# Kernel tuning notes

Hardware: AMD Instinct MI355X
Metric: run time of the kernel (lower is better)

## Reference

```python
import jax, jax.numpy as jnp
import numpy as np

N_NODES = 100000
N_EDGES = 3200000
IN_F = 128


def gcn_conv(x, edge_index, edge_weight, W, b):
    """PyG GCNConv: add self-loops (weight 1), symmetric normalization,
    scatter-add aggregation from src -> dst, then bias."""
    n = x.shape[0]
    src, dst = edge_index[0], edge_index[1]
    h = x @ W  # [N, out]
    # degree with self-loop weight 1
    deg = jax.ops.segment_sum(edge_weight, dst, num_segments=n) + 1.0
    dinv = jax.lax.rsqrt(deg)
    norm = dinv[src] * edge_weight * dinv[dst]  # [E]
    msgs = norm[:, None] * h[src]  # [E, out]
    out = jax.ops.segment_sum(msgs, dst, num_segments=n)
    # self-loop contribution: norm = dinv*1*dinv = 1/deg
    out = out + h / deg[:, None]
    return out + b


def setup_inputs() -> dict:
    key = jax.random.key(0)
    ks = jax.random.split(key, 12)
    x = jax.random.normal(ks[0], (N_NODES, IN_F), dtype=jnp.float32)
    edge_index = jax.random.randint(ks[1], (2, N_EDGES), 0, N_NODES)
    edge_weights = jax.random.uniform(ks[2], (N_EDGES,), dtype=jnp.float32)
    def glorot(k, shape):
        lim = np.sqrt(6.0 / (shape[0] + shape[1]))
        return jax.random.uniform(k, shape, jnp.float32, -lim, lim)
    return {
        "x": x,
        "edge_index": edge_index,
        "edge_weights": edge_weights,
        "W1": glorot(ks[3], (IN_F, 32)),
        "b1": jnp.zeros((32,), jnp.float32),
        "W2": glorot(ks[4], (32, 16)),
        "b2": jnp.zeros((16,), jnp.float32),
        "fc1_w": glorot(ks[5], (16, 1)),
        "fc1_b": jnp.zeros((1,), jnp.float32),
        "fc2_w": glorot(ks[6], (33, 1)),
        "fc2_b": jnp.zeros((1,), jnp.float32),
    }


def reference(x, edge_index, edge_weights, W1, b1, W2, b2, fc1_w, fc1_b, fc2_w, fc2_b):
    x1 = gcn_conv(x, edge_index, edge_weights, W1, b1)
    h = jax.nn.relu(x1)  # dropout is identity in eval mode
    x2 = gcn_conv(h, edge_index, edge_weights, W2, b2)
    x1f = x2 @ fc1_w + fc1_b        # [N, 1]
    c = jax.nn.sigmoid(x1f)
    cat = jnp.concatenate([h, c], axis=1)  # [N, 33]
    r = cat @ fc2_w + fc2_b         # [N, 1]
    return (r, x1f)
```

## Files before the change

kernel.cpp:

```cpp
#include <hip/hip_runtime.h>
#include <math.h>


#define TPB 256
#define PA_CHUNK 4096
#define KMAXB 512
#define NPW 8

__global__ __launch_bounds__(512) void countA_kernel(const int* __restrict__ dst,
                                                     int* __restrict__ gtot,
                                                     int E, int K) {
    __shared__ int lhist[KMAXB];
    const int tid = threadIdx.x;
    const int e0  = blockIdx.x * PA_CHUNK;
    if (tid < KMAXB) lhist[tid] = 0;
    __syncthreads();
#pragma unroll
    for (int i = 0; i < 8; ++i) {
        int e = e0 + tid + i * 512;
        if (e < E) atomicAdd(&lhist[dst[e] >> 8], 1);
    }
    __syncthreads();
    if (tid < K && lhist[tid] > 0) atomicAdd(&gtot[tid], lhist[tid]);
}

__global__ __launch_bounds__(64) void kscan_kernel(const int* __restrict__ gtot,
                                                   int* __restrict__ gstart,
                                                   int* __restrict__ gcursor,
                                                   int K, int E) {
    int tid = threadIdx.x;
    int b0 = tid * 8, v[8], s = 0;
#pragma unroll
    for (int t = 0; t < 8; ++t) {
        v[t] = s;
        int idx = b0 + t;
        s += (idx < K) ? gtot[idx] : 0;
    }
    int incl = s;
#pragma unroll
    for (int d = 1; d < 64; d <<= 1) {
        int t2 = __shfl_up(incl, d);
        if (tid >= d) incl += t2;
    }
    int excl = incl - s;
#pragma unroll
    for (int t = 0; t < 8; ++t) {
        int idx = b0 + t;
        if (idx < K) { gstart[idx] = excl + v[t]; gcursor[idx] = excl + v[t]; }
    }
    if (tid == 63) gstart[K] = E;
}

__global__ __launch_bounds__(512) void placeA_kernel(const int* __restrict__ src,
                                                     const int* __restrict__ dst,
                                                     const float* __restrict__ ew,
                                                     uint2* __restrict__ tmp,
                                                     int* __restrict__ gcursor,
                                                     int E, int K) {
    __shared__ int lhist[KMAXB], lbase[KMAXB], lcur[KMAXB], gbaseS[KMAXB];
    __shared__ int ltot;
    __shared__ uint2 stage[PA_CHUNK];
    __shared__ int   saddr[PA_CHUNK];
    const int tid = threadIdx.x;
    const int e0  = blockIdx.x * PA_CHUNK;

    if (tid < KMAXB) { lhist[tid] = 0; lcur[tid] = 0; }
    __syncthreads();

    int   b[8];
    uint2 p[8];
#pragma unroll
    for (int i = 0; i < 8; ++i) {
        int e = e0 + tid + i * 512;
        b[i] = -1;
        if (e < E) {
            int d   = dst[e];
            int s   = src[e];
            float w = ew[e];
            b[i]   = d >> 8;
            p[i].x = __float_as_uint(w);
            p[i].y = ((unsigned)s << 8) | (unsigned)(d & 255);
            atomicAdd(&lhist[b[i]], 1);
        }
    }
    __syncthreads();

    if (tid < 64) {
        int b0 = tid * 8, v[8], s = 0;
#pragma unroll
        for (int t = 0; t < 8; ++t) { v[t] = s; s += lhist[b0 + t]; }
        int incl = s;
#pragma unroll
        for (int d = 1; d < 64; d <<= 1) {
            int t2 = __shfl_up(incl, d);
            if (tid >= d) incl += t2;
        }
        int excl = incl - s;
#pragma unroll
        for (int t = 0; t < 8; ++t) lbase[b0 + t] = excl + v[t];
        if (tid == 63) ltot = incl;
    }
    __syncthreads();

    if (tid < K && lhist[tid] > 0)
        gbaseS[tid] = atomicAdd(&gcursor[tid], lhist[tid]);
    __syncthreads();

#pragma unroll
    for (int i = 0; i < 8; ++i) {
        if (b[i] >= 0) {
            int r    = atomicAdd(&lcur[b[i]], 1);
            int sidx = lbase[b[i]] + r;
            stage[sidx] = p[i];
            saddr[sidx] = gbaseS[b[i]] + r;
        }
    }
    __syncthreads();

    int tot = ltot;
    for (int s = tid; s < tot; s += 512) tmp[saddr[s]] = stage[s];
}

__global__ __launch_bounds__(512) void partB_kernel(const uint2* __restrict__ tmp,
                                                    const int* __restrict__ gstart,
                                                    int2* __restrict__ epair,
                                                    int* __restrict__ off,
                                                    float* __restrict__ dinv,
                                                    int N) {
    __shared__ int   lhist[256], loff[256], lcur[256];
    __shared__ float ldeg[256];
    const int tid  = threadIdx.x;
    const int k    = blockIdx.x;
    const int seg0 = gstart[k], seg1 = gstart[k + 1];

    if (tid < 256) { lhist[tid] = 0; lcur[tid] = 0; ldeg[tid] = 0.f; }
    __syncthreads();

    for (int j = seg0 + tid; j < seg1; j += 512)
        atomicAdd(&lhist[tmp[j].y & 255u], 1);
    __syncthreads();

    if (tid < 64) {
        int b0 = tid * 4, v[4], s = 0;
#pragma unroll
        for (int t = 0; t < 4; ++t) { v[t] = s; s += lhist[b0 + t]; }
        int incl = s;
#pragma unroll
        for (int d = 1; d < 64; d <<= 1) {
            int t2 = __shfl_up(incl, d);
            if (tid >= d) incl += t2;
        }
        int excl = incl - s;
#pragma unroll
        for (int t = 0; t < 4; ++t) loff[b0 + t] = excl + v[t];
    }
    __syncthreads();

    if (tid < 256) {
        int d = (k << 8) + tid;
        if (d < N) off[d] = seg0 + loff[tid];
    }

    for (int j = seg0 + tid; j < seg1; j += 512) {
        uint2 q  = tmp[j];
        int dlow = q.y & 255u;
        int s    = (int)(q.y >> 8);
        float w  = __uint_as_float(q.x);
        int r    = atomicAdd(&lcur[dlow], 1);
        int2 pr; pr.x = s; pr.y = (int)q.x;
        epair[seg0 + loff[dlow] + r] = pr;
        atomicAdd(&ldeg[dlow], w);
    }
    __syncthreads();

    if (tid < 256) {
        int d = (k << 8) + tid;
        if (d < N) dinv[d] = 1.0f / sqrtf(ldeg[tid] + 1.0f);
    }
}

__global__ __launch_bounds__(TPB) void gemm1_kernel(const float* __restrict__ x,
                                                    const float* __restrict__ W,
                                                    const float* __restrict__ dinv,
                                                    float* __restrict__ h, int N) {
    __shared__ float Ws[128 * 32];
    __shared__ float xs[32 * 129];
    const int tid = threadIdx.x;
    const int nb  = blockIdx.x * 32;

    const float4* W4  = (const float4*)W;
    float4*       Ws4 = (float4*)Ws;
#pragma unroll
    for (int i = 0; i < 4; ++i) Ws4[tid + i * 256] = W4[tid + i * 256];

#pragma unroll
    for (int i = 0; i < 4; ++i) {
        int idx  = tid + i * 256;
        int node = idx >> 5;
        int col4 = idx & 31;
        if (nb + node < N) {
            float4 v = ((const float4*)(x + (size_t)nb * 128))[idx];
            float* p = &xs[node * 129 + col4 * 4];
            p[0] = v.x; p[1] = v.y; p[2] = v.z; p[3] = v.w;
        }
    }
    __syncthreads();

    const int nl = tid >> 3;
    const int og = (tid & 7) * 4;
    float a0 = 0.f, a1 = 0.f, a2 = 0.f, a3 = 0.f;
#pragma unroll 8
    for (int k = 0; k < 128; ++k) {
        float xv = xs[nl * 129 + k];
        const float* wp = &Ws[k * 32 + og];
        a0 = fmaf(xv, wp[0], a0);
        a1 = fmaf(xv, wp[1], a1);
        a2 = fmaf(xv, wp[2], a2);
        a3 = fmaf(xv, wp[3], a3);
    }
    int node = nb + nl;
    if (node < N) {
        float dv = dinv[node];
        float* out = &h[(size_t)node * 32 + og];
        out[0] = a0 * dv; out[1] = a1 * dv; out[2] = a2 * dv; out[3] = a3 * dv;
    }
}

__global__ __launch_bounds__(TPB) void gather32_fused_kernel(
    const int* __restrict__ off, const int2* __restrict__ epair,
    const float* __restrict__ g1, const float* __restrict__ dinv,
    const float* __restrict__ b1, const float* __restrict__ W2,
    const float* __restrict__ fc2_w,
    float* __restrict__ g2, float* __restrict__ rdot, int N, int E) {
    __shared__ float wls[544];
    const int tid = threadIdx.x;
    wls[tid]       = W2[tid];
    wls[tid + 256] = W2[tid + 256];
    if (tid < 32) wls[512 + tid] = fc2_w[tid];
    __syncthreads();

    const int lane = tid & 63;
    const int f    = lane & 31;
    const int half = lane >> 5;
    const float bv = b1[f];
    const int wbase = (lane < 16) ? lane : 512;
    const int wstrd = (lane < 16) ? 16 : 1;

    const int i0 = (blockIdx.x * (TPB / 64) + (tid >> 6)) * NPW;

    for (int t = 0; t < NPW; ++t) {
        int i = i0 + t;
        if (i >= N) return;
        const int s0 = off[i];
        const int s1 = (i + 1 < N) ? off[i + 1] : E;

        float acc = 0.f;
        int j = s0 + half;
        for (; j + 6 < s1; j += 8) {
            int2 pa = epair[j];
            int2 pb = epair[j + 2];
            int2 pc = epair[j + 4];
            int2 pd = epair[j + 6];
            acc = fmaf(__int_as_float(pa.y), g1[(size_t)pa.x * 32 + f], acc);
            acc = fmaf(__int_as_float(pb.y), g1[(size_t)pb.x * 32 + f], acc);
            acc = fmaf(__int_as_float(pc.y), g1[(size_t)pc.x * 32 + f], acc);
            acc = fmaf(__int_as_float(pd.y), g1[(size_t)pd.x * 32 + f], acc);
        }
        for (; j < s1; j += 2) {
            int2 p = epair[j];
            acc = fmaf(__int_as_float(p.y), g1[(size_t)p.x * 32 + f], acc);
        }
        acc += __shfl_xor(acc, 32);

        float dv = dinv[i];
        float v  = fmaxf(dv * (acc + g1[(size_t)i * 32 + f]) + bv, 0.f);

        float hs = 0.f;
#pragma unroll
        for (int k = 0; k < 32; ++k)
            hs = fmaf(__shfl(v, k), wls[wbase + k * wstrd], hs);

        if (lane < 16)       g2[(size_t)i * 16 + lane] = hs * dv;
        else if (lane == 16) rdot[i] = hs;
    }
}

__global__ __launch_bounds__(TPB) void zprep_kernel(const float* __restrict__ g2,
                                                    const float* __restrict__ fc1_w,
                                                    float* __restrict__ z, int N) {
    int i = blockIdx.x * TPB + threadIdx.x;
    if (i >= N) return;
    const float4* g4 = (const float4*)(g2 + (size_t)i * 16);
    float acc = 0.f;
#pragma unroll
    for (int q = 0; q < 4; ++q) {
        float4 v = g4[q];
        acc = fmaf(v.x, fc1_w[q * 4 + 0], acc);
        acc = fmaf(v.y, fc1_w[q * 4 + 1], acc);
        acc = fmaf(v.z, fc1_w[q * 4 + 2], acc);
        acc = fmaf(v.w, fc1_w[q * 4 + 3], acc);
    }
    z[i] = acc;
}

__global__ __launch_bounds__(TPB) void final_scalar_kernel(
    const int* __restrict__ off, const int2* __restrict__ epair,
    const float* __restrict__ z, const float* __restrict__ rdot,
    const float* __restrict__ dinv, const float* __restrict__ b2,
    const float* __restrict__ fc1_w, const float* __restrict__ fc1_b,
    const float* __restrict__ fc2_w, const float* __restrict__ fc2_b,
    float* __restrict__ out, int N, int E) {
    const int tid  = threadIdx.x;
    const int lane = tid & 63;

    float C = fc1_b[0];
#pragma unroll
    for (int f = 0; f < 16; ++f) C = fmaf(b2[f], fc1_w[f], C);
    const float f2w = fc2_w[32];
    const float f2b = fc2_b[0];

    const int i0 = (blockIdx.x * (TPB / 64) + (tid >> 6)) * NPW;

    for (int t = 0; t < NPW; ++t) {
        int i = i0 + t;
        if (i >= N) return;
        const int s0 = off[i];
        const int s1 = (i + 1 < N) ? off[i + 1] : E;

        float acc = 0.f;
        for (int j = s0 + lane; j < s1; j += 64) {
            int2 p = epair[j];
            acc = fmaf(__int_as_float(p.y), z[p.x], acc);
        }
        acc += __shfl_xor(acc, 1);
        acc += __shfl_xor(acc, 2);
        acc += __shfl_xor(acc, 4);
        acc += __shfl_xor(acc, 8);
        acc += __shfl_xor(acc, 16);
        acc += __shfl_xor(acc, 32);

        float x1f = dinv[i] * (acc + z[i]) + C;
        float c   = 1.0f / (1.0f + expf(-x1f));
        float r   = fmaf(c, f2w, f2b) + rdot[i];

        if (lane == 0) {
            out[i]     = r;
            out[N + i] = x1f;
        }
    }
}

extern "C" void kernel_launch(void* const* d_in, const int* in_sizes, int n_in,
                              void* d_out, int out_size, void* d_ws, size_t ws_size,
                              hipStream_t stream) {
    const float* x     = (const float*)d_in[0];
    const int*   ei    = (const int*)d_in[1];
    const float* ew    = (const float*)d_in[2];
    const float* W1    = (const float*)d_in[3];
    const float* b1    = (const float*)d_in[4];
    const float* W2    = (const float*)d_in[5];
    const float* b2    = (const float*)d_in[6];
    const float* fc1_w = (const float*)d_in[7];
    const float* fc1_b = (const float*)d_in[8];
    const float* fc2_w = (const float*)d_in[9];
    const float* fc2_b = (const float*)d_in[10];

    const int N = in_sizes[0] / 128;
    const int E = in_sizes[2];
    const int* src = ei;
    const int* dst = ei + E;
    const int K = (N + 255) >> 8;

    float* ws    = (float*)d_ws;
    float* dinv  = ws;
    float* big   = dinv + N;
    float* g1    = big;
    float* g2    = big + (size_t)32 * N;
    float* rdot  = big + (size_t)48 * N;
    float* z     = big + (size_t)49 * N;
    int*   off   = (int*)(big + (size_t)64 * N);
    int2*  epair = (int2*)(off + N);
    int*   gcursor = (int*)(epair + E);
    int*   gstart  = gcursor + K;
    uint2* tmp   = (uint2*)big;

    size_t need = ((size_t)66 * N + (size_t)2 * E + 2 * K + 2) * 4;
    if (ws_size < need || K > KMAXB || (size_t)E > (size_t)32 * N) return;

    hipMemsetAsync(gcursor, 0, (size_t)K * sizeof(int), stream);

    countA_kernel<<<(E + PA_CHUNK - 1) / PA_CHUNK, 512, 0, stream>>>(dst, gcursor, E, K);
    kscan_kernel<<<1, 64, 0, stream>>>(gcursor, gstart, gcursor, K, E);
    placeA_kernel<<<(E + PA_CHUNK - 1) / PA_CHUNK, 512, 0, stream>>>(
        src, dst, ew, tmp, gcursor, E, K);
    partB_kernel<<<K, 512, 0, stream>>>(tmp, gstart, epair, off, dinv, N);

    gemm1_kernel<<<(N + 31) / 32, TPB, 0, stream>>>(x, W1, dinv, g1, N);

    const int gblocks = (N + 4 * NPW - 1) / (4 * NPW);
    gather32_fused_kernel<<<gblocks, TPB, 0, stream>>>(
        off, epair, g1, dinv, b1, W2, fc2_w, g2, rdot, N, E);
    zprep_kernel<<<(N + TPB - 1) / TPB, TPB, 0, stream>>>(g2, fc1_w, z, N);
    final_scalar_kernel<<<gblocks, TPB, 0, stream>>>(
        off, epair, z, rdot, dinv, b2, fc1_w, fc1_b, fc2_w, fc2_b,
        (float*)d_out, N, E);
}
```

Measured before the change: 345.1 us.

## Widen CSR bucket to 512 destinations and unroll aggregation loop to 16

Changes the two-pass counting sort to use 512-destination buckets instead of 256, so there are half as many buckets (K~196) and each partB block handles 512 nodes with all threads active. It also unrolls the layer-1 gather/aggregate loop to 16 edges per iteration to keep more independent loads in flight. The risks are fewer partB blocks (less parallelism), heavier per-block shared-memory atomics, source index packing now limited to 23 bits, and higher register pressure in the aggregation kernel.

```diff
diff --git a/kernel.cpp b/kernel.cpp
--- a/kernel.cpp
+++ b/kernel.cpp
@@ -5,6 +5,8 @@
 #define TPB 256
 #define PA_CHUNK 4096
 #define KMAXB 512
+#define BSH 9
+#define BMSK 511
 #define NPW 8
 
 __global__ __launch_bounds__(512) void countA_kernel(const int* __restrict__ dst,
@@ -18,7 +20,7 @@
 #pragma unroll
     for (int i = 0; i < 8; ++i) {
         int e = e0 + tid + i * 512;
-        if (e < E) atomicAdd(&lhist[dst[e] >> 8], 1);
+        if (e < E) atomicAdd(&lhist[dst[e] >> BSH], 1);
     }
     __syncthreads();
     if (tid < K && lhist[tid] > 0) atomicAdd(&gtot[tid], lhist[tid]);
@@ -77,9 +79,9 @@
             int d   = dst[e];
             int s   = src[e];
             float w = ew[e];
-            b[i]   = d >> 8;
+            b[i]   = d >> BSH;
             p[i].x = __float_as_uint(w);
-            p[i].y = ((unsigned)s << 8) | (unsigned)(d & 255);
+            p[i].y = ((unsigned)s << BSH) | (unsigned)(d & BMSK);
             atomicAdd(&lhist[b[i]], 1);
         }
     }
@@ -127,23 +129,23 @@
                                                     int* __restrict__ off,
                                                     float* __restrict__ dinv,
                                                     int N) {
-    __shared__ int   lhist[256], loff[256], lcur[256];
-    __shared__ float ldeg[256];
+    __shared__ int   lhist[512], loff[512], lcur[512];
+    __shared__ float ldeg[512];
     const int tid  = threadIdx.x;
     const int k    = blockIdx.x;
     const int seg0 = gstart[k], seg1 = gstart[k + 1];
 
-    if (tid < 256) { lhist[tid] = 0; lcur[tid] = 0; ldeg[tid] = 0.f; }
+    lhist[tid] = 0; lcur[tid] = 0; ldeg[tid] = 0.f;
     __syncthreads();
 
     for (int j = seg0 + tid; j < seg1; j += 512)
-        atomicAdd(&lhist[tmp[j].y & 255u], 1);
+        atomicAdd(&lhist[tmp[j].y & (unsigned)BMSK], 1);
     __syncthreads();
 
     if (tid < 64) {
-        int b0 = tid * 4, v[4], s = 0;
-#pragma unroll
-        for (int t = 0; t < 4; ++t) { v[t] = s; s += lhist[b0 + t]; }
+        int b0 = tid * 8, v[8], s = 0;
+#pragma unroll
+        for (int t = 0; t < 8; ++t) { v[t] = s; s += lhist[b0 + t]; }
         int incl = s;
 #pragma unroll
         for (int d = 1; d < 64; d <<= 1) {
@@ -152,19 +154,19 @@
         }
         int excl = incl - s;
 #pragma unroll
-        for (int t = 0; t < 4; ++t) loff[b0 + t] = excl + v[t];
-    }
-    __syncthreads();
-
-    if (tid < 256) {
-        int d = (k << 8) + tid;
+        for (int t = 0; t < 8; ++t) loff[b0 + t] = excl + v[t];
+    }
+    __syncthreads();
+
+    {
+        int d = (k << BSH) + tid;
         if (d < N) off[d] = seg0 + loff[tid];
     }
 
     for (int j = seg0 + tid; j < seg1; j += 512) {
         uint2 q  = tmp[j];
-        int dlow = q.y & 255u;
-        int s    = (int)(q.y >> 8);
+        int dlow = q.y & (unsigned)BMSK;
+        int s    = (int)(q.y >> BSH);
         float w  = __uint_as_float(q.x);
         int r    = atomicAdd(&lcur[dlow], 1);
         int2 pr; pr.x = s; pr.y = (int)q.x;
@@ -173,8 +175,8 @@
     }
     __syncthreads();
 
-    if (tid < 256) {
-        int d = (k << 8) + tid;
+    {
+        int d = (k << BSH) + tid;
         if (d < N) dinv[d] = 1.0f / sqrtf(ldeg[tid] + 1.0f);
     }
 }
@@ -256,15 +258,23 @@
 
         float acc = 0.f;
         int j = s0 + half;
-        for (; j + 6 < s1; j += 8) {
+        for (; j + 14 < s1; j += 16) {
             int2 pa = epair[j];
             int2 pb = epair[j + 2];
             int2 pc = epair[j + 4];
             int2 pd = epair[j + 6];
+            int2 pe = epair[j + 8];
+            int2 pf = epair[j + 10];
+            int2 pg = epair[j + 12];
+            int2 ph = epair[j + 14];
             acc = fmaf(__int_as_float(pa.y), g1[(size_t)pa.x * 32 + f], acc);
             acc = fmaf(__int_as_float(pb.y), g1[(size_t)pb.x * 32 + f], acc);
             acc = fmaf(__int_as_float(pc.y), g1[(size_t)pc.x * 32 + f], acc);
             acc = fmaf(__int_as_float(pd.y), g1[(size_t)pd.x * 32 + f], acc);
+            acc = fmaf(__int_as_float(pe.y), g1[(size_t)pe.x * 32 + f], acc);
+            acc = fmaf(__int_as_float(pf.y), g1[(size_t)pf.x * 32 + f], acc);
+            acc = fmaf(__int_as_float(pg.y), g1[(size_t)pg.x * 32 + f], acc);
+            acc = fmaf(__int_as_float(ph.y), g1[(size_t)ph.x * 32 + f], acc);
         }
         for (; j < s1; j += 2) {
             int2 p = epair[j];
@@ -369,7 +379,7 @@
     const int E = in_sizes[2];
     const int* src = ei;
     const int* dst = ei + E;
-    const int K = (N + 255) >> 8;
+    const int K = (N + BMSK) >> BSH;
 
     float* ws    = (float*)d_ws;
     float* dinv  = ws;
```

New measurement: 376.1 us. 9.0% more time.
